# Optimization experiments

Measured on AMD Instinct MI355X. Metric: run time of the kernel, lower is better.

The kernel has to match this reference:

```python
import jax, jax.numpy as jnp
import numpy as np
from jax import lax

B, T = 64, 2048
ENC, DEC, ATT = 512, 1024, 128
NFILT, KSIZE = 32, 31
PAD = KSIZE // 2


def setup_inputs() -> dict:
    key = jax.random.key(0)
    ks = jax.random.split(key, 9)
    query = jax.random.normal(ks[0], (B, 1, DEC), dtype=jnp.float32)
    keys = jax.random.normal(ks[1], (B, T, ENC), dtype=jnp.float32)
    prev_weights = jax.random.uniform(ks[2], (B, T), dtype=jnp.float32)
    mask = jax.random.randint(ks[3], (B, T), 0, 2, dtype=jnp.int32)
    # params stored as [in, out] (transpose of torch Linear weight); same math
    W1 = jax.random.normal(ks[4], (ENC, ATT), dtype=jnp.float32) * (ENC ** -0.5)
    W2 = jax.random.normal(ks[5], (DEC, ATT), dtype=jnp.float32) * (DEC ** -0.5)
    V = jax.random.normal(ks[6], (ATT,), dtype=jnp.float32) * (ATT ** -0.5)
    conv_w = jax.random.normal(ks[7], (NFILT, 1, KSIZE), dtype=jnp.float32) * (KSIZE ** -0.5)
    loc_dense = jax.random.normal(ks[8], (NFILT, ATT), dtype=jnp.float32) * (NFILT ** -0.5)
    return {"query": query, "keys": keys, "prev_weights": prev_weights, "mask": mask,
            "W1": W1, "W2": W2, "V": V, "conv_w": conv_w, "loc_dense": loc_dense}


def reference(query, keys, prev_weights, mask, W1, W2, V, conv_w, loc_dense):
    proj_key = jnp.einsum('bte,ea->bta', keys, W1)          # [B,T,A]
    proj_query = jnp.einsum('bqd,da->bqa', query, W2)       # [B,1,A]
    # location conv: input [B,1,T], kernel [F,1,K], 'same' padding -> [B,F,T]
    loc_feat = lax.conv_general_dilated(prev_weights[:, None, :], conv_w,
                                        window_strides=(1,), padding=[(PAD, PAD)],
                                        dimension_numbers=('NCH', 'OIH', 'NCH'))
    proj_loc = jnp.einsum('bft,fa->bta', loc_feat, loc_dense)  # [B,T,A]
    scores = jnp.einsum('bta,a->bt', jnp.tanh(proj_key + proj_query + proj_loc), V)
    scores = jnp.where(mask == 0, -1e9, scores)
    weights = jax.nn.softmax(scores, axis=-1)                # [B,T]
    context = jnp.einsum('bt,bte->be', weights, keys)[:, None, :]  # [B,1,ENC]
    return context, weights
```

## Files before the change

### kernel.cpp

```cpp
#include <hip/hip_runtime.h>

typedef __attribute__((ext_vector_type(4))) float f32x4;
typedef __attribute__((ext_vector_type(2))) float f32x2;
typedef __attribute__((ext_vector_type(8))) short bf16x8;

#define T_LEN 2048
#define ENC   512
#define DEC   1024
#define ATT   128
#define NB    64
#define BM    128
#define BK    32
#define NXB   (T_LEN / BM)

typedef unsigned int u32;
typedef __attribute__((address_space(1))) const u32 gu32;
typedef __attribute__((address_space(3))) u32 lu32;

__device__ __forceinline__ void async_copy16(const void* g, void* l) {
  __builtin_amdgcn_global_load_lds((gu32*)g, (lu32*)l, 16, 0, 0);
}

__device__ __forceinline__ unsigned short f2bf_rne(float x) {
  unsigned int u = __builtin_bit_cast(unsigned int, x);
  u += 0x7fff + ((u >> 16) & 1);
  return (unsigned short)(u >> 16);
}
__device__ __forceinline__ short f2bf_fast(float x) {
  unsigned int u = __builtin_bit_cast(unsigned int, x);
  return (short)((u + 0x8000u) >> 16);
}

__device__ __forceinline__ float fast_tanh(float x) {
  float e = __expf(2.f * x);
  return 1.f - 2.f / (e + 1.f);
}

__global__ __launch_bounds__(128) void prep(
    const float* __restrict__ query, const float* __restrict__ W2,
    const float* __restrict__ W1, const float* __restrict__ convw,
    const float* __restrict__ ldense,
    float* __restrict__ pq, unsigned short* __restrict__ Bl) {
  int bidx = blockIdx.x;
  if (bidx < NB) {
    int a = threadIdx.x;
    const float* q = query + bidx * DEC;
    float a0 = 0.f, a1 = 0.f, a2 = 0.f, a3 = 0.f;
    for (int d = 0; d < DEC; d += 4) {
      a0 += q[d]     * W2[(d)     * ATT + a];
      a1 += q[d + 1] * W2[(d + 1) * ATT + a];
      a2 += q[d + 2] * W2[(d + 2) * ATT + a];
      a3 += q[d + 3] * W2[(d + 3) * ATT + a];
    }
    pq[bidx * ATT + a] = (a0 + a1) + (a2 + a3);
  } else {
    int a = bidx - NB;
    for (int k = threadIdx.x; k < 17 * BK; k += 128) {
      float v = 0.f;
      if (k < 512) {
        v = W1[k * ATT + a];
      } else if (k < 543) {
        int kc = k - 512;
        #pragma unroll
        for (int f = 0; f < 32; ++f) v += convw[f * 31 + kc] * ldense[f * ATT + a];
      }
      int kt = k >> 5, kk = k & 31;
      Bl[(((kt * 4) + (kk >> 3)) * 128 + a) * 8 + (kk & 7)] = f2bf_rne(v);
    }
  }
}

__global__ __launch_bounds__(256, 2) void lsa_main(
    const float* __restrict__ keys, const float* __restrict__ prev,
    const int* __restrict__ mask, const unsigned short* __restrict__ Bl,
    const float* __restrict__ pq, const float* __restrict__ Vv,
    float* __restrict__ wout, float* __restrict__ dpart, float* __restrict__ cpart) {
  __shared__ float Abuf[3][BM * BK];
  __shared__ unsigned short Bbuf[3][ATT * BK];
  __shared__ float s_red[2][BM];
  __shared__ float e_vals[BM];

  const int tid = threadIdx.x;
  const int b = blockIdx.y;
  const int trow0 = blockIdx.x * BM;
  const int bid = b * NXB + blockIdx.x;

  const int lane = tid & 63;
  const int w = tid >> 6;
  const int wr = w >> 1, wc = w & 1;
  const int rsel = lane & 15, grp = lane >> 4;

  const int lr = lane >> 3, cp = lane & 7;
  const int gc = cp ^ lr;
  const float* gA = keys + ((size_t)b * T_LEN + trow0 + w * 32 + lr) * ENC + gc * 4;

  const int rx = rsel & 7;
  const int ca0 = (2 * grp) ^ rx, ca1 = (2 * grp + 1) ^ rx;
  const int arow_base = (wr * 64 + rsel) * BK;

  const int bcol_base = wc * 64 + rsel;

  f32x4 acc[4][4];
  #pragma unroll
  for (int m = 0; m < 4; ++m)
    #pragma unroll
    for (int n = 0; n < 4; ++n) acc[m][n] = (f32x4)0.f;

  auto STAGE = [&](int t, int buf) {
    const float* gt = gA + t * BK;
    float* dstA = &Abuf[buf][0];
    #pragma unroll
    for (int i = 0; i < 4; ++i)
      async_copy16(gt + (size_t)i * 8 * ENC, &dstA[(w * 4 + i) * 256]);
    const unsigned short* gBt = Bl + (size_t)t * (ATT * BK) + w * 1024 + lane * 8;
    unsigned short* dstB = &Bbuf[buf][0];
    #pragma unroll
    for (int j = 0; j < 2; ++j)
      async_copy16(gBt + j * 512, &dstB[w * 1024 + j * 512]);
  };

  auto COMPUTE = [&](int buf) {
    const unsigned short* Bb = &Bbuf[buf][0];
    bf16x8 bfr[4];
    #pragma unroll
    for (int n = 0; n < 4; ++n)
      bfr[n] = *reinterpret_cast<const bf16x8*>(&Bb[(grp * 128 + bcol_base + n * 16) * 8]);
    const float* Ab = &Abuf[buf][0];
    #pragma unroll
    for (int m = 0; m < 4; ++m) {
      f32x4 x0 = *reinterpret_cast<const f32x4*>(&Ab[arow_base + m * 16 * BK + ca0 * 4]);
      f32x4 x1 = *reinterpret_cast<const f32x4*>(&Ab[arow_base + m * 16 * BK + ca1 * 4]);
      bf16x8 af;
      #pragma unroll
      for (int j = 0; j < 4; ++j) { af[j] = f2bf_fast(x0[j]); af[4 + j] = f2bf_fast(x1[j]); }
      #pragma unroll
      for (int n = 0; n < 4; ++n)
        acc[m][n] = __builtin_amdgcn_mfma_f32_16x16x32_bf16(af, bfr[n], acc[m][n], 0, 0, 0);
    }
  };

  STAGE(0, 0);
  STAGE(1, 1);
  asm volatile("s_waitcnt vmcnt(6)" ::: "memory");
  __builtin_amdgcn_s_barrier();
  __builtin_amdgcn_sched_barrier(0);

  #pragma unroll
  for (int t = 0; t < 14; ++t) {
    STAGE(t + 2, (t + 2) % 3);
    COMPUTE(t % 3);
    asm volatile("s_waitcnt vmcnt(6)" ::: "memory");
    __builtin_amdgcn_s_barrier();
    __builtin_amdgcn_sched_barrier(0);
  }

  {
    const unsigned short* gBt = Bl + (size_t)16 * (ATT * BK) + w * 1024 + lane * 8;
    unsigned short* dstB = &Bbuf[1][0];
    #pragma unroll
    for (int j = 0; j < 2; ++j)
      async_copy16(gBt + j * 512, &dstB[w * 1024 + j * 512]);
    const int r_ = tid >> 1, kh_ = tid & 1;
    const int rx2_ = r_ & 7;
    float* dstA = &Abuf[1][r_ * BK];
    #pragma unroll
    for (int jc = 0; jc < 4; ++jc) {
      int c = kh_ * 4 + jc;
      f32x4 v;
      #pragma unroll
      for (int q = 0; q < 4; ++q) {
        int kk = c * 4 + q;
        int pos = trow0 + r_ + kk - 15;
        v[q] = (kk < 31 && pos >= 0 && pos < T_LEN) ? prev[b * T_LEN + pos] : 0.f;
      }
      *reinterpret_cast<f32x4*>(&dstA[(c ^ rx2_) * 4]) = v;
    }
    COMPUTE(14 % 3);
    __syncthreads();
  }

  COMPUTE(15 % 3);
  COMPUTE(16 % 3);

  float psum[4][4];
  #pragma unroll
  for (int m = 0; m < 4; ++m)
    #pragma unroll
    for (int i = 0; i < 4; ++i) psum[m][i] = 0.f;
  #pragma unroll
  for (int n = 0; n < 4; ++n) {
    int c = wc * 64 + n * 16 + rsel;
    float pqv = pq[b * ATT + c];
    float vv = Vv[c];
    #pragma unroll
    for (int m = 0; m < 4; ++m)
      #pragma unroll
      for (int i = 0; i < 4; ++i)
        psum[m][i] += vv * fast_tanh(acc[m][n][i] + pqv);
  }
  #pragma unroll
  for (int m = 0; m < 4; ++m)
    #pragma unroll
    for (int i = 0; i < 4; ++i) {
      float v = psum[m][i];
      v += __shfl_xor(v, 1, 64);
      v += __shfl_xor(v, 2, 64);
      v += __shfl_xor(v, 4, 64);
      v += __shfl_xor(v, 8, 64);
      psum[m][i] = v;
    }
  if (rsel == 0) {
    #pragma unroll
    for (int m = 0; m < 4; ++m)
      #pragma unroll
      for (int i = 0; i < 4; ++i)
        s_red[wc][wr * 64 + m * 16 + grp * 4 + i] = psum[m][i];
  }
  __syncthreads();

  if (tid < BM) {
    int trow = trow0 + tid;
    float s = s_red[0][tid] + s_red[1][tid];
    float e = (mask[b * T_LEN + trow] == 0) ? 0.f : __expf(s);
    wout[b * T_LEN + trow] = e;
    e_vals[tid] = e;
  }
  __syncthreads();

  if (tid < 64) {
    float v = e_vals[tid] + e_vals[tid + 64];
    #pragma unroll
    for (int off = 32; off; off >>= 1) v += __shfl_xor(v, off, 64);
    if (tid == 0) dpart[bid] = v;
  }

  {
    const float* kcol = keys + ((size_t)b * T_LEN + trow0) * ENC + 2 * tid;
    f32x2 cacc; cacc.x = 0.f; cacc.y = 0.f;
    #pragma unroll 8
    for (int r = 0; r < BM; ++r) {
      float e = e_vals[r];
      f32x2 kv = *reinterpret_cast<const f32x2*>(kcol + (size_t)r * ENC);
      cacc.x += e * kv.x;
      cacc.y += e * kv.y;
    }
    *reinterpret_cast<f32x2*>(cpart + (size_t)bid * ENC + 2 * tid) = cacc;
  }
}

__global__ __launch_bounds__(256) void lsa_finalize(
    const float* __restrict__ dpart, const float* __restrict__ cpart,
    float* __restrict__ out) {
  int b = blockIdx.x, tid = threadIdx.x;
  float d = 0.f;
  #pragma unroll
  for (int i = 0; i < NXB; ++i) d += dpart[b * NXB + i];
  float inv = 1.f / d;
  for (int e = tid; e < ENC; e += 256) {
    float c = 0.f;
    #pragma unroll
    for (int i = 0; i < NXB; ++i) c += cpart[((size_t)(b * NXB + i)) * ENC + e];
    out[b * ENC + e] = c * inv;
  }
  float* wrow = out + NB * ENC + (size_t)b * T_LEN;
  for (int t = tid; t < T_LEN; t += 256) wrow[t] *= inv;
}

extern "C" void kernel_launch(void* const* d_in, const int* in_sizes, int n_in,
                              void* d_out, int out_size, void* d_ws, size_t ws_size,
                              hipStream_t stream) {
  const float* query  = (const float*)d_in[0];
  const float* keys   = (const float*)d_in[1];
  const float* prev   = (const float*)d_in[2];
  const int*   mask   = (const int*)d_in[3];
  const float* W1     = (const float*)d_in[4];
  const float* W2     = (const float*)d_in[5];
  const float* V      = (const float*)d_in[6];
  const float* convw  = (const float*)d_in[7];
  const float* ldense = (const float*)d_in[8];
  float* out = (float*)d_out;

  char* ws = (char*)d_ws;
  unsigned short* Bl = (unsigned short*)ws;
  float* pq    = (float*)(ws + 139264);
  float* dpart = (float*)(ws + 139264 + 32768);
  float* cpart = (float*)(ws + 139264 + 32768 + 4096);

  prep<<<dim3(192), dim3(128), 0, stream>>>(query, W2, W1, convw, ldense, pq, Bl);
  dim3 grid(NXB, NB);
  lsa_main<<<grid, dim3(256), 0, stream>>>(keys, prev, mask, Bl, pq, V,
                                           out + NB * ENC, dpart, cpart);
  lsa_finalize<<<dim3(NB), dim3(256), 0, stream>>>(dpart, cpart, out);
}
```

Before: 130.0 us.

## Load full projection matrix into LDS once and stream keys directly into registers

```diff
diff --git a/kernel.cpp b/kernel.cpp
--- a/kernel.cpp
+++ b/kernel.cpp
@@ -1,7 +1,6 @@
 #include <hip/hip_runtime.h>
 
 typedef __attribute__((ext_vector_type(4))) float f32x4;
-typedef __attribute__((ext_vector_type(2))) float f32x2;
 typedef __attribute__((ext_vector_type(8))) short bf16x8;
 
 #define T_LEN 2048
@@ -9,9 +8,9 @@
 #define DEC   1024
 #define ATT   128
 #define NB    64
-#define BM    128
-#define BK    32
-#define NXB   (T_LEN / BM)
+#define BM    256
+#define NTB   (T_LEN / BM)
+#define NSTEP 17
 
 typedef unsigned int u32;
 typedef __attribute__((address_space(1))) const u32 gu32;
@@ -55,7 +54,8 @@
     pq[bidx * ATT + a] = (a0 + a1) + (a2 + a3);
   } else {
     int a = bidx - NB;
-    for (int k = threadIdx.x; k < 17 * BK; k += 128) {
+    int n = a >> 4, rs = a & 15;
+    for (int k = threadIdx.x; k < NSTEP * 32; k += 128) {
       float v = 0.f;
       if (k < 512) {
         v = W1[k * ATT + a];
@@ -64,142 +64,110 @@
         #pragma unroll
         for (int f = 0; f < 32; ++f) v += convw[f * 31 + kc] * ldense[f * ATT + a];
       }
-      int kt = k >> 5, kk = k & 31;
-      Bl[(((kt * 4) + (kk >> 3)) * 128 + a) * 8 + (kk & 7)] = f2bf_rne(v);
-    }
-  }
-}
-
-__global__ __launch_bounds__(256, 2) void lsa_main(
+      int t = k >> 5, g = (k & 31) >> 3, j = k & 7;
+      Bl[(((t * 8 + n) * 64 + g * 16 + rs) << 3) + j] = f2bf_rne(v);
+    }
+  }
+}
+
+__global__ __launch_bounds__(512, 2) void lsa_main(
     const float* __restrict__ keys, const float* __restrict__ prev,
     const int* __restrict__ mask, const unsigned short* __restrict__ Bl,
     const float* __restrict__ pq, const float* __restrict__ Vv,
     float* __restrict__ wout, float* __restrict__ dpart, float* __restrict__ cpart) {
-  __shared__ float Abuf[3][BM * BK];
-  __shared__ unsigned short Bbuf[3][ATT * BK];
-  __shared__ float s_red[2][BM];
+  __shared__ unsigned short Bsh[NSTEP * 4096];
   __shared__ float e_vals[BM];
 
   const int tid = threadIdx.x;
-  const int b = blockIdx.y;
-  const int trow0 = blockIdx.x * BM;
-  const int bid = b * NXB + blockIdx.x;
-
+  const int bid = blockIdx.x;
+  const int b = bid >> 3;
+  const int trow0 = (bid & 7) * BM;
   const int lane = tid & 63;
   const int w = tid >> 6;
-  const int wr = w >> 1, wc = w & 1;
   const int rsel = lane & 15, grp = lane >> 4;
-
-  const int lr = lane >> 3, cp = lane & 7;
-  const int gc = cp ^ lr;
-  const float* gA = keys + ((size_t)b * T_LEN + trow0 + w * 32 + lr) * ENC + gc * 4;
-
-  const int rx = rsel & 7;
-  const int ca0 = (2 * grp) ^ rx, ca1 = (2 * grp + 1) ^ rx;
-  const int arow_base = (wr * 64 + rsel) * BK;
-
-  const int bcol_base = wc * 64 + rsel;
-
-  f32x4 acc[4][4];
-  #pragma unroll
-  for (int m = 0; m < 4; ++m)
-    #pragma unroll
-    for (int n = 0; n < 4; ++n) acc[m][n] = (f32x4)0.f;
-
-  auto STAGE = [&](int t, int buf) {
-    const float* gt = gA + t * BK;
-    float* dstA = &Abuf[buf][0];
-    #pragma unroll
-    for (int i = 0; i < 4; ++i)
-      async_copy16(gt + (size_t)i * 8 * ENC, &dstA[(w * 4 + i) * 256]);
-    const unsigned short* gBt = Bl + (size_t)t * (ATT * BK) + w * 1024 + lane * 8;
-    unsigned short* dstB = &Bbuf[buf][0];
-    #pragma unroll
-    for (int j = 0; j < 2; ++j)
-      async_copy16(gBt + j * 512, &dstB[w * 1024 + j * 512]);
-  };
-
-  auto COMPUTE = [&](int buf) {
-    const unsigned short* Bb = &Bbuf[buf][0];
-    bf16x8 bfr[4];
-    #pragma unroll
-    for (int n = 0; n < 4; ++n)
-      bfr[n] = *reinterpret_cast<const bf16x8*>(&Bb[(grp * 128 + bcol_base + n * 16) * 8]);
-    const float* Ab = &Abuf[buf][0];
-    #pragma unroll
-    for (int m = 0; m < 4; ++m) {
-      f32x4 x0 = *reinterpret_cast<const f32x4*>(&Ab[arow_base + m * 16 * BK + ca0 * 4]);
-      f32x4 x1 = *reinterpret_cast<const f32x4*>(&Ab[arow_base + m * 16 * BK + ca1 * 4]);
-      bf16x8 af;
-      #pragma unroll
-      for (int j = 0; j < 4; ++j) { af[j] = f2bf_fast(x0[j]); af[4 + j] = f2bf_fast(x1[j]); }
-      #pragma unroll
-      for (int n = 0; n < 4; ++n)
-        acc[m][n] = __builtin_amdgcn_mfma_f32_16x16x32_bf16(af, bfr[n], acc[m][n], 0, 0, 0);
-    }
-  };
-
-  STAGE(0, 0);
-  STAGE(1, 1);
-  asm volatile("s_waitcnt vmcnt(6)" ::: "memory");
-  __builtin_amdgcn_s_barrier();
-  __builtin_amdgcn_sched_barrier(0);
-
-  #pragma unroll
-  for (int t = 0; t < 14; ++t) {
-    STAGE(t + 2, (t + 2) % 3);
-    COMPUTE(t % 3);
-    asm volatile("s_waitcnt vmcnt(6)" ::: "memory");
-    __builtin_amdgcn_s_barrier();
+  const int row0 = trow0 + w * 32;
+
+  const float* keyrow = keys + ((size_t)b * T_LEN + row0 + rsel) * ENC + grp * 8;
+
+  f32x4 acc[2][8];
+  #pragma unroll
+  for (int m = 0; m < 2; ++m)
+    #pragma unroll
+    for (int n = 0; n < 8; ++n) acc[m][n] = (f32x4)0.f;
+
+  f32x4 aP[2][2], aQ[2][2];
+  #pragma unroll
+  for (int m = 0; m < 2; ++m) {
+    aP[m][0] = *(const f32x4*)(keyrow + m * 16 * ENC);
+    aP[m][1] = *(const f32x4*)(keyrow + m * 16 * ENC + 4);
+  }
+  {
+    const char* src = (const char*)Bl + w * 1024 + lane * 16;
+    char* dst = (char*)Bsh + w * 1024;
+    #pragma unroll
+    for (int s = 0; s < NSTEP; ++s)
+      async_copy16(src + s * 8192, dst + s * 8192);
+  }
+  __syncthreads();
+
+  #pragma unroll
+  for (int t = 0; t < NSTEP; ++t) {
+    f32x4 (&cur)[2][2] = (t & 1) ? aQ : aP;
+    f32x4 (&nxt)[2][2] = (t & 1) ? aP : aQ;
+    if (t < NSTEP - 2) {
+      #pragma unroll
+      for (int m = 0; m < 2; ++m) {
+        nxt[m][0] = *(const f32x4*)(keyrow + m * 16 * ENC + (t + 1) * 32);
+        nxt[m][1] = *(const f32x4*)(keyrow + m * 16 * ENC + (t + 1) * 32 + 4);
+      }
+    } else if (t == NSTEP - 2) {
+      #pragma unroll
+      for (int m = 0; m < 2; ++m)
+        #pragma unroll
+        for (int h = 0; h < 2; ++h)
+          #pragma unroll
+          for (int j = 0; j < 4; ++j) {
+            int kk = grp * 8 + h * 4 + j;
+            int pos = row0 + m * 16 + rsel + kk - 15;
+            nxt[m][h][j] = (kk < 31 && pos >= 0 && pos < T_LEN) ? prev[b * T_LEN + pos] : 0.f;
+          }
+    }
     __builtin_amdgcn_sched_barrier(0);
-  }
-
-  {
-    const unsigned short* gBt = Bl + (size_t)16 * (ATT * BK) + w * 1024 + lane * 8;
-    unsigned short* dstB = &Bbuf[1][0];
-    #pragma unroll
-    for (int j = 0; j < 2; ++j)
-      async_copy16(gBt + j * 512, &dstB[w * 1024 + j * 512]);
-    const int r_ = tid >> 1, kh_ = tid & 1;
-    const int rx2_ = r_ & 7;
-    float* dstA = &Abuf[1][r_ * BK];
-    #pragma unroll
-    for (int jc = 0; jc < 4; ++jc) {
-      int c = kh_ * 4 + jc;
-      f32x4 v;
-      #pragma unroll
-      for (int q = 0; q < 4; ++q) {
-        int kk = c * 4 + q;
-        int pos = trow0 + r_ + kk - 15;
-        v[q] = (kk < 31 && pos >= 0 && pos < T_LEN) ? prev[b * T_LEN + pos] : 0.f;
-      }
-      *reinterpret_cast<f32x4*>(&dstA[(c ^ rx2_) * 4]) = v;
-    }
-    COMPUTE(14 % 3);
-    __syncthreads();
-  }
-
-  COMPUTE(15 % 3);
-  COMPUTE(16 % 3);
-
-  float psum[4][4];
-  #pragma unroll
-  for (int m = 0; m < 4; ++m)
+    bf16x8 af[2];
+    #pragma unroll
+    for (int m = 0; m < 2; ++m)
+      #pragma unroll
+      for (int j = 0; j < 4; ++j) {
+        af[m][j]     = f2bf_fast(cur[m][0][j]);
+        af[m][4 + j] = f2bf_fast(cur[m][1][j]);
+      }
+    const unsigned short* Bt = &Bsh[t * 4096];
+    #pragma unroll
+    for (int n = 0; n < 8; ++n) {
+      bf16x8 bf = *(const bf16x8*)(Bt + n * 512 + lane * 8);
+      acc[0][n] = __builtin_amdgcn_mfma_f32_16x16x32_bf16(af[0], bf, acc[0][n], 0, 0, 0);
+      acc[1][n] = __builtin_amdgcn_mfma_f32_16x16x32_bf16(af[1], bf, acc[1][n], 0, 0, 0);
+    }
+  }
+
+  float psum[2][4];
+  #pragma unroll
+  for (int m = 0; m < 2; ++m)
     #pragma unroll
     for (int i = 0; i < 4; ++i) psum[m][i] = 0.f;
   #pragma unroll
-  for (int n = 0; n < 4; ++n) {
-    int c = wc * 64 + n * 16 + rsel;
+  for (int n = 0; n < 8; ++n) {
+    int c = n * 16 + rsel;
     float pqv = pq[b * ATT + c];
     float vv = Vv[c];
     #pragma unroll
-    for (int m = 0; m < 4; ++m)
+    for (int m = 0; m < 2; ++m)
       #pragma unroll
       for (int i = 0; i < 4; ++i)
         psum[m][i] += vv * fast_tanh(acc[m][n][i] + pqv);
   }
   #pragma unroll
-  for (int m = 0; m < 4; ++m)
+  for (int m = 0; m < 2; ++m)
     #pragma unroll
     for (int i = 0; i < 4; ++i) {
       float v = psum[m][i];
@@ -211,40 +179,32 @@
     }
   if (rsel == 0) {
     #pragma unroll
-    for (int m = 0; m < 4; ++m)
-      #pragma unroll
-      for (int i = 0; i < 4; ++i)
-        s_red[wc][wr * 64 + m * 16 + grp * 4 + i] = psum[m][i];
+    for (int m = 0; m < 2; ++m)
+      #pragma unroll
+      for (int i = 0; i < 4; ++i) {
+        int r = w * 32 + m * 16 + grp * 4 + i;
+        int gr = b * T_LEN + trow0 + r;
+        float e = (mask[gr] == 0) ? 0.f : __expf(psum[m][i]);
+        wout[gr] = e;
+        e_vals[r] = e;
+      }
   }
   __syncthreads();
 
-  if (tid < BM) {
-    int trow = trow0 + tid;
-    float s = s_red[0][tid] + s_red[1][tid];
-    float e = (mask[b * T_LEN + trow] == 0) ? 0.f : __expf(s);
-    wout[b * T_LEN + trow] = e;
-    e_vals[tid] = e;
-  }
-  __syncthreads();
-
   if (tid < 64) {
-    float v = e_vals[tid] + e_vals[tid + 64];
+    float v = e_vals[tid] + e_vals[tid + 64] + e_vals[tid + 128] + e_vals[tid + 192];
     #pragma unroll
     for (int off = 32; off; off >>= 1) v += __shfl_xor(v, off, 64);
     if (tid == 0) dpart[bid] = v;
   }
 
   {
-    const float* kcol = keys + ((size_t)b * T_LEN + trow0) * ENC + 2 * tid;
-    f32x2 cacc; cacc.x = 0.f; cacc.y = 0.f;
-    #pragma unroll 8
-    for (int r = 0; r < BM; ++r) {
-      float e = e_vals[r];
-      f32x2 kv = *reinterpret_cast<const f32x2*>(kcol + (size_t)r * ENC);
-      cacc.x += e * kv.x;
-      cacc.y += e * kv.y;
-    }
-    *reinterpret_cast<f32x2*>(cpart + (size_t)bid * ENC + 2 * tid) = cacc;
+    float c = 0.f;
+    const float* kb = keys + ((size_t)b * T_LEN + trow0) * ENC + tid;
+    #pragma unroll 16
+    for (int r = 0; r < BM; ++r)
+      c += e_vals[r] * kb[(size_t)r * ENC];
+    cpart[(size_t)bid * ENC + tid] = c;
   }
 }
 
@@ -254,12 +214,12 @@
   int b = blockIdx.x, tid = threadIdx.x;
   float d = 0.f;
   #pragma unroll
-  for (int i = 0; i < NXB; ++i) d += dpart[b * NXB + i];
+  for (int i = 0; i < NTB; ++i) d += dpart[b * NTB + i];
   float inv = 1.f / d;
   for (int e = tid; e < ENC; e += 256) {
     float c = 0.f;
     #pragma unroll
-    for (int i = 0; i < NXB; ++i) c += cpart[((size_t)(b * NXB + i)) * ENC + e];
+    for (int i = 0; i < NTB; ++i) c += cpart[((size_t)(b * NTB + i)) * ENC + e];
     out[b * ENC + e] = c * inv;
   }
   float* wrow = out + NB * ENC + (size_t)b * T_LEN;
@@ -287,8 +247,7 @@
   float* cpart = (float*)(ws + 139264 + 32768 + 4096);
 
   prep<<<dim3(192), dim3(128), 0, stream>>>(query, W2, W1, convw, ldense, pq, Bl);
-  dim3 grid(NXB, NB);
-  lsa_main<<<grid, dim3(256), 0, stream>>>(keys, prev, mask, Bl, pq, V,
-                                           out + NB * ENC, dpart, cpart);
+  lsa_main<<<dim3(NB * NTB), dim3(512), 0, stream>>>(keys, prev, mask, Bl, pq, V,
+                                                     out + NB * ENC, dpart, cpart);
   lsa_finalize<<<dim3(NB), dim3(256), 0, stream>>>(dpart, cpart, out);
 }
```

Result: slower. 136.2 us (+4.7%).
